# Kernel optimization log

Measured on AMD Instinct MI355X. Metric: run time of the kernel, lower is better.

Reference implementation:

```python
import jax, jax.numpy as jnp
import numpy as np

NUM_HEADS = 16
HEAD_DIM = 128
QUERY_DIM = 2048
SCALE = HEAD_DIM ** -0.5


def setup_inputs() -> dict:
    key = jax.random.key(0)
    ks = jax.random.split(key, 11)
    B, L, D = 2, 2048, QUERY_DIM
    HD = NUM_HEADS * HEAD_DIM
    s = 0.02
    return {
        "x_q": jax.random.normal(ks[0], (B, L, D), jnp.float32),
        "x_k": jax.random.normal(ks[1], (B, L, D), jnp.float32),
        "x_v": jax.random.normal(ks[2], (B, L, D), jnp.float32),
        "Wq": jax.random.normal(ks[3], (D, HD), jnp.float32) * s,
        "bq": jnp.zeros((HD,), jnp.float32),
        "Wk": jax.random.normal(ks[4], (D, HD), jnp.float32) * s,
        "bk": jnp.zeros((HD,), jnp.float32),
        "Wv": jax.random.normal(ks[5], (D, HD), jnp.float32) * s,
        "bv": jnp.zeros((HD,), jnp.float32),
        "Wo": jax.random.normal(ks[6], (HD, D), jnp.float32) * s,
        "bo": jnp.zeros((D,), jnp.float32),
    }


def _split_heads(x):  # [b, l, h*d] -> [b, h, l, d]
    b, l, _ = x.shape
    return x.reshape(b, l, NUM_HEADS, HEAD_DIM).transpose(0, 2, 1, 3)


def reference(x_q, x_k, x_v, Wq, bq, Wk, bk, Wv, bv, Wo, bo):
    # Note: the torch module constructs norm_q/norm_k but NEVER applies them in forward.
    q = _split_heads(x_q @ Wq + bq)  # [b, h, l, d]
    k = _split_heads(x_k @ Wk + bk)
    v = _split_heads(x_v @ Wv + bv)
    scores = jnp.einsum("bhid,bhjd->bhij", q, k) * SCALE
    probs = jax.nn.softmax(scores, axis=-1)
    o = jnp.einsum("bhij,bhjd->bhid", probs, v)  # [b, h, l, d]
    b, h, l, d = o.shape
    o = o.transpose(0, 2, 1, 3).reshape(b, l, h * d)
    return o @ Wo + bo
```

## Files before the change

### kernel.cpp

```cpp
#include <hip/hip_runtime.h>


typedef _Float16 f16;
typedef __attribute__((ext_vector_type(8))) _Float16 f16x8;
typedef __attribute__((ext_vector_type(4))) _Float16 f16x4;
typedef __attribute__((ext_vector_type(4))) float f32x4;
typedef __attribute__((ext_vector_type(4))) unsigned int u32x4;

#define QSCALE (0.08838834764831845f * 1.4426950408889634f)
#define SWZ3(r) (((r) & 3) | (((r) >> 1) & 4))
#define SWZV(r) ((r) & 7)

static __device__ __forceinline__ void gload16(void* lds, const void* g) {
  __builtin_amdgcn_global_load_lds(
      (__attribute__((address_space(1))) void*)g,
      (__attribute__((address_space(3))) void*)lds, 16, 0, 0);
}

__global__ __launch_bounds__(256) void cvt_x_kernel(
    const float* __restrict__ x0, const float* __restrict__ x1,
    const float* __restrict__ x2, f16* __restrict__ out) {
  const float* x = blockIdx.z == 0 ? x0 : (blockIdx.z == 1 ? x1 : x2);
  f16* o = out + (size_t)blockIdx.z * 8388608;
  size_t i = ((size_t)blockIdx.x * 256 + threadIdx.x) * 8;
  f32x4 a = *(const f32x4*)(x + i);
  f32x4 b = *(const f32x4*)(x + i + 4);
  f16x8 r;
  r[0] = (f16)a[0]; r[1] = (f16)a[1]; r[2] = (f16)a[2]; r[3] = (f16)a[3];
  r[4] = (f16)b[0]; r[5] = (f16)b[1]; r[6] = (f16)b[2]; r[7] = (f16)b[3];
  *(f16x8*)(o + i) = r;
}

__global__ __launch_bounds__(256) void cvt_w_kernel(
    const float* __restrict__ w0, const float* __restrict__ w1,
    const float* __restrict__ w2, const float* __restrict__ w3,
    f16* __restrict__ out) {
  const float* W = blockIdx.z == 0 ? w0 : blockIdx.z == 1 ? w1
                 : blockIdx.z == 2 ? w2 : w3;
  f16* WT = out + (size_t)blockIdx.z * 4194304;
  __shared__ f16 tile[64][68];
  const int tx = threadIdx.x & 15, ty = threadIdx.x >> 4;
  const int k0 = blockIdx.y * 64, n0 = blockIdx.x * 64;
#pragma unroll
  for (int i = 0; i < 4; ++i) {
    int r = ty + i * 16;
    f32x4 v = *(const f32x4*)(W + (size_t)(k0 + r) * 2048 + n0 + tx * 4);
    tile[r][tx * 4 + 0] = (f16)v[0]; tile[r][tx * 4 + 1] = (f16)v[1];
    tile[r][tx * 4 + 2] = (f16)v[2]; tile[r][tx * 4 + 3] = (f16)v[3];
  }
  __syncthreads();
#pragma unroll
  for (int i = 0; i < 4; ++i) {
    int n = ty + i * 16;
    f16x4 o;
    o[0] = tile[tx * 4 + 0][n]; o[1] = tile[tx * 4 + 1][n];
    o[2] = tile[tx * 4 + 2][n]; o[3] = tile[tx * 4 + 3][n];
    *(f16x4*)(WT + (size_t)(n0 + n) * 2048 + k0 + tx * 4) = o;
  }
}

__global__ __launch_bounds__(512, 2) void gemm_qkv_kernel(
    const f16* __restrict__ Abase, const f16* __restrict__ Btbase,
    f16* __restrict__ Obase, const float* __restrict__ b0,
    const float* __restrict__ b1, const float* __restrict__ b2) {
  const int z = blockIdx.z;
  const f16* A  = Abase  + (size_t)z * 8388608;
  const f16* Bt = Btbase + (size_t)z * 4194304;
  f16* Oz = Obase + (size_t)z * 8388608;
  const float* bias = z == 0 ? b0 : z == 1 ? b1 : b2;
  const float qsc = z == 0 ? QSCALE : 1.0f;
  const int tid = threadIdx.x, lane = tid & 63, w = tid >> 6;
  const int wm = w >> 2, wn = w & 3;
  const int bm = blockIdx.y, bn = blockIdx.x;
  const int l15 = lane & 15, lg = lane >> 4;
  __shared__ alignas(16) char smb[131072];

  f32x4 acc[8][4];
#pragma unroll
  for (int i = 0; i < 8; ++i)
#pragma unroll
    for (int j = 0; j < 4; ++j) acc[i][j] = (f32x4)0.f;

#define GSTAGE(KT, C_)                                                        \
  {                                                                           \
    char* Ab_ = smb + (C_) * 65536;                                           \
    char* Bb_ = Ab_ + 32768;                                                  \
    _Pragma("unroll") for (int p = 0; p < 4; ++p) {                           \
      int L = p * 8192 + tid * 16;                                            \
      int row = L >> 7, pcol = L & 127;                                       \
      int scol = pcol ^ ((row & 7) << 4);                                     \
      gload16(Ab_ + L,                                                        \
              (const char*)A + ((size_t)(bm * 256 + row) * 2048 + (KT) * 64) * 2 + scol); \
      gload16(Bb_ + L,                                                        \
              (const char*)Bt + ((size_t)(bn * 256 + row) * 2048 + (KT) * 64) * 2 + scol); \
    }                                                                         \
  }

  GSTAGE(0, 0);
#pragma unroll 1
  for (int kt = 0; kt < 32; ++kt) {
    const int c = kt & 1;
    if (kt < 31) {
      GSTAGE(kt + 1, c ^ 1);
      asm volatile("s_waitcnt vmcnt(8)" ::: "memory");
    } else {
      asm volatile("s_waitcnt vmcnt(0)" ::: "memory");
    }
    __builtin_amdgcn_s_barrier();

    const char* Ab = smb + c * 65536;
    const char* Bb = Ab + 32768;
    f16x8 bf[4][2];
#pragma unroll
    for (int p = 0; p < 4; ++p) {
      f16x8 af[2][2];
#pragma unroll
      for (int pp = 0; pp < 2; ++pp)
#pragma unroll
        for (int h = 0; h < 2; ++h) {
          int row = wm * 128 + (p * 2 + pp) * 16 + l15;
          af[pp][h] = *(const f16x8*)(Ab + row * 128 +
                                      ((h * 64 + lg * 16) ^ ((row & 7) << 4)));
        }
      if (p == 0) {
#pragma unroll
        for (int j = 0; j < 4; ++j)
#pragma unroll
          for (int h = 0; h < 2; ++h) {
            int row = wn * 64 + j * 16 + l15;
            bf[j][h] = *(const f16x8*)(Bb + row * 128 +
                                       ((h * 64 + lg * 16) ^ ((row & 7) << 4)));
          }
      }
      __builtin_amdgcn_s_setprio(1);
#pragma unroll
      for (int pp = 0; pp < 2; ++pp)
#pragma unroll
        for (int j = 0; j < 4; ++j)
#pragma unroll
          for (int h = 0; h < 2; ++h)
            acc[p * 2 + pp][j] = __builtin_amdgcn_mfma_f32_16x16x32_f16(
                af[pp][h], bf[j][h], acc[p * 2 + pp][j], 0, 0, 0);
      __builtin_amdgcn_s_setprio(0);
      __builtin_amdgcn_s_barrier();
    }
  }

#pragma unroll
  for (int i = 0; i < 8; ++i)
#pragma unroll
    for (int j = 0; j < 4; ++j) {
      int col = bn * 256 + wn * 64 + j * 16 + l15;
      int h = col >> 7, d = col & 127;
      float bv = bias[col];
#pragma unroll
      for (int r = 0; r < 4; ++r) {
        int rowg = bm * 256 + wm * 128 + i * 16 + lg * 4 + r;
        int b_ = rowg >> 11, lpos = rowg & 2047;
        Oz[(size_t)(b_ * 16 + h) * 262144 + (size_t)lpos * 128 + d] =
            (f16)((acc[i][j][r] + bv) * qsc);
      }
    }
#undef GSTAGE
}

__global__ __launch_bounds__(256) void gemm_out_kernel(
    const f16* __restrict__ A, const f16* __restrict__ Bt,
    float* __restrict__ Out, const float* __restrict__ bias) {
  const int tid = threadIdx.x, lane = tid & 63, w = tid >> 6;
  const int wm = w >> 1, wn = w & 1;
  const int bm = blockIdx.y, bn = blockIdx.x;
  const int l15 = lane & 15, lg = lane >> 4;
  __shared__ alignas(16) f16 As[128 * 32];
  __shared__ alignas(16) f16 Bs[128 * 32];
  f32x4 acc[4][4];
#pragma unroll
  for (int i = 0; i < 4; ++i)
#pragma unroll
    for (int j = 0; j < 4; ++j) acc[i][j] = (f32x4)0.f;

  for (int kt = 0; kt < 64; ++kt) {
    __syncthreads();
#pragma unroll
    for (int i = 0; i < 2; ++i) {
      int c = i * 4 + w;
      int phys = c * 1024 + lane * 16;
      int row = phys >> 6, colb = phys & 63;
      gload16((char*)As + c * 1024,
              (const char*)A + ((size_t)(bm * 128 + row) * 2048 + kt * 32) * 2 + colb);
      gload16((char*)Bs + c * 1024,
              (const char*)Bt + ((size_t)(bn * 128 + row) * 2048 + kt * 32) * 2 + colb);
    }
    __syncthreads();
    f16x8 af[4], bf[4];
#pragma unroll
    for (int i = 0; i < 4; ++i)
      af[i] = *(const f16x8*)(As + (wm * 64 + i * 16 + l15) * 32 + lg * 8);
#pragma unroll
    for (int j = 0; j < 4; ++j)
      bf[j] = *(const f16x8*)(Bs + (wn * 64 + j * 16 + l15) * 32 + lg * 8);
#pragma unroll
    for (int i = 0; i < 4; ++i)
#pragma unroll
      for (int j = 0; j < 4; ++j)
        acc[i][j] = __builtin_amdgcn_mfma_f32_16x16x32_f16(af[i], bf[j], acc[i][j], 0, 0, 0);
  }
#pragma unroll
  for (int i = 0; i < 4; ++i)
#pragma unroll
    for (int j = 0; j < 4; ++j) {
      int col = bn * 128 + wn * 64 + j * 16 + l15;
      float bv = bias[col];
#pragma unroll
      for (int r = 0; r < 4; ++r) {
        int rowg = bm * 128 + wm * 64 + i * 16 + lg * 4 + r;
        Out[(size_t)rowg * 2048 + col] = acc[i][j][r] + bv;
      }
    }
}

__global__ __launch_bounds__(256) void tr_v_kernel(const f16* __restrict__ v,
                                                   f16* __restrict__ vtout) {
  const int bh = blockIdx.z;
  const f16* V = v + (size_t)bh * 262144;
  f16* VT = vtout + (size_t)bh * 262144;
  __shared__ f16 tile[64][68];
  const int tx = threadIdx.x & 15, ty = threadIdx.x >> 4;
  const int l0 = blockIdx.x * 64, d0 = blockIdx.y * 64;
#pragma unroll
  for (int i = 0; i < 4; ++i) {
    int r = ty + i * 16;
    f16x4 val = *(const f16x4*)(V + (size_t)(l0 + r) * 128 + d0 + tx * 4);
    tile[r][tx * 4 + 0] = val[0]; tile[r][tx * 4 + 1] = val[1];
    tile[r][tx * 4 + 2] = val[2]; tile[r][tx * 4 + 3] = val[3];
  }
  __syncthreads();
#pragma unroll
  for (int i = 0; i < 4; ++i) {
    int d = ty + i * 16;
    f16x4 o;
    o[0] = tile[tx * 4 + 0][d]; o[1] = tile[tx * 4 + 1][d];
    o[2] = tile[tx * 4 + 2][d]; o[3] = tile[tx * 4 + 3][d];
    *(f16x4*)(VT + (size_t)(d0 + d) * 2048 + l0 + tx * 4) = o;
  }
}

__global__ __launch_bounds__(512, 4) void attn_kernel(
    const f16* __restrict__ q, const f16* __restrict__ k,
    const f16* __restrict__ vt, f16* __restrict__ o) {
  const int orig = blockIdx.y * 16 + blockIdx.x;
  const int swz = (orig & 7) * 64 + (orig >> 3);
  const int qt = swz & 15, bh = swz >> 4;
  const int tid = threadIdx.x, lane = tid & 63, w = tid >> 6;
  const int l15 = lane & 15, lg = lane >> 4;
  const f16* Qb = q + (size_t)bh * 262144 + (size_t)qt * 128 * 128;
  const char* Kb = (const char*)(k + (size_t)bh * 262144);
  const char* Vtb = (const char*)(vt + (size_t)bh * 262144);
  __shared__ alignas(16) char sm[65536];

  f16x8 qf[4];
#pragma unroll
  for (int ks = 0; ks < 4; ++ks)
    qf[ks] = *(const f16x8*)(Qb + (w * 16 + l15) * 128 + ks * 32 + lg * 8);

  f32x4 oacc[8];
#pragma unroll
  for (int df = 0; df < 8; ++df) oacc[df] = (f32x4)0.f;
  float mrow = -1e30f, ps = 0.f;
  const int rA = ((l15 >> 2) << 3) + (l15 & 3);

#define STAGE(T, B)                                                          \
  {                                                                          \
    char* Ks_ = sm + (B) * 32768;                                            \
    char* Vs_ = Ks_ + 16384;                                                 \
    _Pragma("unroll") for (int i = 0; i < 2; ++i) {                          \
      int c = i * 8 + w;                                                     \
      int phys = c * 1024 + lane * 16;                                       \
      {                                                                      \
        int row = phys >> 8, pcol = phys & 255;                              \
        int lcol = pcol ^ (SWZ3(row) << 4);                                  \
        gload16(Ks_ + c * 1024, Kb + (size_t)((T) * 64 + row) * 256 + lcol); \
      }                                                                      \
      {                                                                      \
        int row = phys >> 7, pcol = phys & 127;                              \
        int lcol = pcol ^ (SWZV(row) << 4);                                  \
        gload16(Vs_ + c * 1024, Vtb + (size_t)row * 4096 + (T) * 128 + lcol);\
      }                                                                      \
    }                                                                        \
  }

  STAGE(0, 0);
  int cur = 0;
  for (int t = 0; t < 32; ++t) {
    __syncthreads();
    if (t < 31) STAGE(t + 1, cur ^ 1);
    const char* Ks = sm + cur * 32768;
    const char* Vs = Ks + 16384;

    f32x4 s[4];
#pragma unroll
    for (int nf = 0; nf < 4; ++nf) s[nf] = (f32x4)0.f;
    __builtin_amdgcn_s_setprio(1);
#pragma unroll
    for (int ks = 0; ks < 4; ++ks) {
      f16x8 kf[4];
#pragma unroll
      for (int nf = 0; nf < 4; ++nf) {
        int row = ((nf & 1) << 5) + ((nf >> 1) << 2) + rA;
        int colb = (ks * 64 + lg * 16) ^ (SWZ3(row) << 4);
        kf[nf] = *(const f16x8*)(Ks + row * 256 + colb);
      }
#pragma unroll
      for (int nf = 0; nf < 4; ++nf)
        s[nf] = __builtin_amdgcn_mfma_f32_16x16x32_f16(kf[nf], qf[ks], s[nf], 0, 0, 0);
    }
    __builtin_amdgcn_s_setprio(0);

    unsigned int pk[2][4];
    {
      float m0 = fmaxf(fmaxf(s[0][0], s[0][1]), fmaxf(s[0][2], s[0][3]));
      float m1 = fmaxf(fmaxf(s[1][0], s[1][1]), fmaxf(s[1][2], s[1][3]));
      float m2 = fmaxf(fmaxf(s[2][0], s[2][1]), fmaxf(s[2][2], s[2][3]));
      float m3 = fmaxf(fmaxf(s[3][0], s[3][1]), fmaxf(s[3][2], s[3][3]));
      float mx = fmaxf(fmaxf(m0, m1), fmaxf(m2, m3));
      mx = fmaxf(mx, __shfl_xor(mx, 16));
      mx = fmaxf(mx, __shfl_xor(mx, 32));
      if (!__all(mx <= mrow + 8.f)) {
        float mnew = fmaxf(mrow, mx);
        float sc = exp2f(mrow - mnew);
        mrow = mnew;
        ps *= sc;
#pragma unroll
        for (int r = 0; r < 4; ++r) {
          float scr = __shfl(sc, (lane & 48) | (lg * 4 + r));
#pragma unroll
          for (int df = 0; df < 8; ++df) oacc[df][r] *= scr;
        }
      }
      float m = mrow;
      float psum = 0.f;
#pragma unroll
      for (int nf = 0; nf < 4; ++nf)
#pragma unroll
        for (int h = 0; h < 2; ++h) {
          float p0 = exp2f(s[nf][2 * h] - m);
          float p1 = exp2f(s[nf][2 * h + 1] - m);
          psum += p0 + p1;
          pk[nf & 1][(nf >> 1) * 2 + h] =
              __builtin_bit_cast(unsigned int, __builtin_amdgcn_cvt_pkrtz(p0, p1));
        }
      ps += psum;
    }

    __builtin_amdgcn_s_setprio(1);
#pragma unroll
    for (int kvs = 0; kvs < 2; ++kvs) {
      f16x8 pa = __builtin_bit_cast(f16x8, *(const u32x4*)pk[kvs]);
#pragma unroll
      for (int df = 0; df < 8; ++df) {
        int row = df * 16 + l15;
        int colb = (kvs * 64 + lg * 16) ^ (SWZV(row) << 4);
        f16x8 vb = *(const f16x8*)(Vs + row * 128 + colb);
        oacc[df] = __builtin_amdgcn_mfma_f32_16x16x32_f16(pa, vb, oacc[df], 0, 0, 0);
      }
    }
    __builtin_amdgcn_s_setprio(0);
    cur ^= 1;
  }

  const int b_ = bh >> 4, h_ = bh & 15;
  f16* Ob = o + (size_t)b_ * 4194304 + (size_t)qt * 128 * 2048 + h_ * 128;
  float lr = ps;
  lr += __shfl_xor(lr, 16);
  lr += __shfl_xor(lr, 32);
  float inv = 1.f / lr;
#pragma unroll
  for (int r = 0; r < 4; ++r) {
    float invr = __shfl(inv, (lane & 48) | (lg * 4 + r));
    int rl = w * 16 + lg * 4 + r;
#pragma unroll
    for (int df = 0; df < 8; ++df)
      Ob[(size_t)rl * 2048 + df * 16 + l15] = (f16)(oacc[df][r] * invr);
  }
#undef STAGE
}

extern "C" void kernel_launch(void* const* d_in, const int* in_sizes, int n_in,
                              void* d_out, int out_size, void* d_ws, size_t ws_size,
                              hipStream_t stream) {
  const float* xq = (const float*)d_in[0];
  const float* xk = (const float*)d_in[1];
  const float* xv = (const float*)d_in[2];
  const float* Wq = (const float*)d_in[3];
  const float* bq = (const float*)d_in[4];
  const float* Wk = (const float*)d_in[5];
  const float* bk = (const float*)d_in[6];
  const float* Wv = (const float*)d_in[7];
  const float* bv = (const float*)d_in[8];
  const float* Wo = (const float*)d_in[9];
  const float* bo = (const float*)d_in[10];

  char* ws = (char*)d_ws;
  f16* xh   = (f16*)(ws);
  f16* wt   = (f16*)(ws + 50331648);
  f16* qkv  = (f16*)(ws + 83886080);
  f16* vtb  = (f16*)(ws);
  f16* oatt = (f16*)(ws + 16777216);
  float* outp = (float*)d_out;

  hipLaunchKernelGGL(cvt_x_kernel, dim3(4096, 1, 3), dim3(256), 0, stream,
                     xq, xk, xv, xh);
  hipLaunchKernelGGL(cvt_w_kernel, dim3(32, 32, 4), dim3(256), 0, stream,
                     Wq, Wk, Wv, Wo, wt);
  hipLaunchKernelGGL(gemm_qkv_kernel, dim3(8, 16, 3), dim3(512), 0, stream,
                     xh, wt, qkv, bq, bk, bv);
  hipLaunchKernelGGL(tr_v_kernel, dim3(32, 2, 32), dim3(256), 0, stream,
                     qkv + (size_t)2 * 8388608, vtb);
  hipLaunchKernelGGL(attn_kernel, dim3(16, 32), dim3(512), 0, stream,
                     qkv, qkv + (size_t)8388608, vtb, oatt);
  hipLaunchKernelGGL(gemm_out_kernel, dim3(16, 32), dim3(256), 0, stream,
                     oatt, wt + (size_t)3 * 4194304, outp, bo);
}
```

Measured before the change: 321.1 us.

## Software-pipeline LDS fragment reads in QKV GEMM and remap blocks across XCDs

The QKV projection GEMM now double-buffers its A-fragment registers, issuing LDS reads for the next sub-tile while MFMAs run on the current one. Explicit waitcnt and sched_barrier calls keep the compiler from reordering that interleave. The grid is flattened to 1D, and block IDs are remapped so that consecutive tiles land on the same XCD, which should improve L2 reuse of A and B tiles. The extra fragment registers raise register pressure, which could hurt the 2-blocks-per-CU occupancy target.

```diff
diff --git a/kernel.cpp b/kernel.cpp
--- a/kernel.cpp
+++ b/kernel.cpp
@@ -63,7 +63,9 @@
     const f16* __restrict__ Abase, const f16* __restrict__ Btbase,
     f16* __restrict__ Obase, const float* __restrict__ b0,
     const float* __restrict__ b1, const float* __restrict__ b2) {
-  const int z = blockIdx.z;
+  const int lid = blockIdx.x;
+  const int logi = (lid & 7) * 48 + (lid >> 3);
+  const int bn = logi & 7, bm = (logi >> 3) & 15, z = logi >> 7;
   const f16* A  = Abase  + (size_t)z * 8388608;
   const f16* Bt = Btbase + (size_t)z * 4194304;
   f16* Oz = Obase + (size_t)z * 8388608;
@@ -71,7 +73,6 @@
   const float qsc = z == 0 ? QSCALE : 1.0f;
   const int tid = threadIdx.x, lane = tid & 63, w = tid >> 6;
   const int wm = w >> 2, wn = w & 3;
-  const int bm = blockIdx.y, bn = blockIdx.x;
   const int l15 = lane & 15, lg = lane >> 4;
   __shared__ alignas(16) char smb[131072];
 
@@ -96,6 +97,23 @@
     }                                                                         \
   }
 
+#define GREADS(P)                                                             \
+  _Pragma("unroll") for (int pp = 0; pp < 2; ++pp)                            \
+    _Pragma("unroll") for (int h = 0; h < 2; ++h) {                           \
+      int row = wm * 128 + ((P) * 2 + pp) * 16 + l15;                         \
+      af[(P) & 1][pp][h] = *(const f16x8*)(                                   \
+          Ab + row * 128 + ((h * 64 + lg * 16) ^ ((row & 7) << 4)));          \
+    }
+
+#define GMFMA(P)                                                              \
+  __builtin_amdgcn_s_setprio(1);                                              \
+  _Pragma("unroll") for (int pp = 0; pp < 2; ++pp)                            \
+    _Pragma("unroll") for (int j = 0; j < 4; ++j)                             \
+      _Pragma("unroll") for (int h = 0; h < 2; ++h)                           \
+        acc[(P) * 2 + pp][j] = __builtin_amdgcn_mfma_f32_16x16x32_f16(        \
+            af[(P) & 1][pp][h], bf[j][h], acc[(P) * 2 + pp][j], 0, 0, 0);     \
+  __builtin_amdgcn_s_setprio(0);
+
   GSTAGE(0, 0);
 #pragma unroll 1
   for (int kt = 0; kt < 32; ++kt) {
@@ -110,40 +128,37 @@
 
     const char* Ab = smb + c * 65536;
     const char* Bb = Ab + 32768;
-    f16x8 bf[4][2];
-#pragma unroll
-    for (int p = 0; p < 4; ++p) {
-      f16x8 af[2][2];
-#pragma unroll
-      for (int pp = 0; pp < 2; ++pp)
-#pragma unroll
-        for (int h = 0; h < 2; ++h) {
-          int row = wm * 128 + (p * 2 + pp) * 16 + l15;
-          af[pp][h] = *(const f16x8*)(Ab + row * 128 +
-                                      ((h * 64 + lg * 16) ^ ((row & 7) << 4)));
-        }
-      if (p == 0) {
-#pragma unroll
-        for (int j = 0; j < 4; ++j)
-#pragma unroll
-          for (int h = 0; h < 2; ++h) {
-            int row = wn * 64 + j * 16 + l15;
-            bf[j][h] = *(const f16x8*)(Bb + row * 128 +
-                                       ((h * 64 + lg * 16) ^ ((row & 7) << 4)));
-          }
-      }
-      __builtin_amdgcn_s_setprio(1);
-#pragma unroll
-      for (int pp = 0; pp < 2; ++pp)
-#pragma unroll
-        for (int j = 0; j < 4; ++j)
-#pragma unroll
-          for (int h = 0; h < 2; ++h)
-            acc[p * 2 + pp][j] = __builtin_amdgcn_mfma_f32_16x16x32_f16(
-                af[pp][h], bf[j][h], acc[p * 2 + pp][j], 0, 0, 0);
-      __builtin_amdgcn_s_setprio(0);
-      __builtin_amdgcn_s_barrier();
-    }
+    f16x8 af[2][2][2], bf[4][2];
+    GREADS(0);
+#pragma unroll
+    for (int j = 0; j < 4; ++j)
+#pragma unroll
+      for (int h = 0; h < 2; ++h) {
+        int row = wn * 64 + j * 16 + l15;
+        bf[j][h] = *(const f16x8*)(Bb + row * 128 +
+                                   ((h * 64 + lg * 16) ^ ((row & 7) << 4)));
+      }
+    asm volatile("s_waitcnt lgkmcnt(0)" ::: "memory");
+    __builtin_amdgcn_sched_barrier(0);
+    GMFMA(0);
+    GREADS(1);
+    __builtin_amdgcn_sched_barrier(0);
+    __builtin_amdgcn_s_barrier();
+    asm volatile("s_waitcnt lgkmcnt(0)" ::: "memory");
+    __builtin_amdgcn_sched_barrier(0);
+    GMFMA(1);
+    GREADS(2);
+    __builtin_amdgcn_sched_barrier(0);
+    __builtin_amdgcn_s_barrier();
+    asm volatile("s_waitcnt lgkmcnt(0)" ::: "memory");
+    __builtin_amdgcn_sched_barrier(0);
+    GMFMA(2);
+    GREADS(3);
+    __builtin_amdgcn_sched_barrier(0);
+    __builtin_amdgcn_s_barrier();
+    asm volatile("s_waitcnt lgkmcnt(0)" ::: "memory");
+    __builtin_amdgcn_sched_barrier(0);
+    GMFMA(3);
   }
 
 #pragma unroll
@@ -162,6 +177,8 @@
       }
     }
 #undef GSTAGE
+#undef GREADS
+#undef GMFMA
 }
 
 __global__ __launch_bounds__(256) void gemm_out_kernel(
@@ -412,7 +429,7 @@
                      xq, xk, xv, xh);
   hipLaunchKernelGGL(cvt_w_kernel, dim3(32, 32, 4), dim3(256), 0, stream,
                      Wq, Wk, Wv, Wo, wt);
-  hipLaunchKernelGGL(gemm_qkv_kernel, dim3(8, 16, 3), dim3(512), 0, stream,
+  hipLaunchKernelGGL(gemm_qkv_kernel, dim3(384, 1, 1), dim3(512), 0, stream,
                      xh, wt, qkv, bq, bk, bv);
   hipLaunchKernelGGL(tr_v_kernel, dim3(32, 2, 32), dim3(256), 0, stream,
                      qkv + (size_t)2 * 8388608, vtb);
```

Result: faster. 310.7 us (-3.2%).
